# Performance work log

Hardware: AMD Instinct MI355X
Metric: run time of the kernel (lower is better)

The kernel has to match this reference:

```python
import jax, jax.numpy as jnp
import numpy as np

N_NODES, N_EDGES, BATCH_SIZE = 8192, 65536, 64
N_S, NG, MAX_R = 16, 32, 10.0
SQRT3 = float(np.sqrt(3.0))


def _mlp2(h, w1, b1, w2, b2):
    return jax.nn.relu(h @ w1 + b1) @ w2 + b2


def _mlp3(h, w1, b1, w2, b2, w3, b3):
    h = jax.nn.relu(h @ w1 + b1)
    h = jax.nn.relu(h @ w2 + b2)
    return h @ w3 + b3


def _scatter_mean(vals, idx, n):
    s = jax.ops.segment_sum(vals, idx, num_segments=n)
    c = jax.ops.segment_sum(jnp.ones(vals.shape[:1], vals.dtype), idx, num_segments=n)
    return s / jnp.maximum(c, 1.0)[:, None]


def _forward_molecule(x, pos, src, dst, batch, params):
    (ne_w1, ne_b1, ne_w2, ne_b2, ee_w1, ee_b1, ee_w2, ee_b2,
     c0_w1, c0_b1, c0_w2, c0_b2, c1_w1, c1_b1, c1_w2, c1_b2,
     sn_w1, sn_b1, sn_w2, sn_b2, sn_w3, sn_b3,
     se_w1, se_b1, se_w2, se_b2, se_w3, se_b3) = params
    n = x.shape[0]
    evec = pos[dst] - pos[src]                       # [E,3]
    dist = jnp.sqrt(jnp.sum(evec * evec, -1) + 1e-12)
    mu = jnp.linspace(0.0, MAX_R, NG)
    coeff = -0.5 / (MAX_R / (NG - 1)) ** 2           # GaussianSmearing
    edge_attr = jnp.exp(coeff * (dist[:, None] - mu) ** 2)     # [E,NG]
    sh1 = SQRT3 * evec / dist[:, None]               # l=1 SH, component norm; l=0 part == 1

    h = _mlp2(x, ne_w1, ne_b1, ne_w2, ne_b2)         # node embedding [N,16]
    eemb = _mlp2(edge_attr, ee_w1, ee_b1, ee_w2, ee_b2)        # edge embedding [E,16]

    # ---- conv 0: 16x0e (x) 0e+1o -> 16x0e+16x1o, per-edge TP weights ----
    ea = jnp.concatenate([eemb, h[dst, :N_S], h[src, :N_S]], -1)   # [E,48]
    w = _mlp2(ea, c0_w1, c0_b1, c0_w2, c0_b2)                      # [E,512]
    E = w.shape[0]
    w00 = w[:, :256].reshape(E, 16, 16)    # 0e x 0e -> 0e
    w01 = w[:, 256:].reshape(E, 16, 16)    # 0e x 1o -> 1o
    xs = h[src]
    o0 = 0.25 * jnp.einsum('eu,euw->ew', xs, w00)        # path weight 1/sqrt(16)
    o1 = 0.25 * jnp.einsum('eu,em,euw->ewm', xs, sh1, w01)
    tp = jnp.concatenate([o0, o1.reshape(E, 48)], -1)
    up = _scatter_mean(tp, dst, n)                       # [N,64]
    h = jnp.pad(h, ((0, 0), (0, up.shape[1] - h.shape[1]))) + up

    # ---- conv 1: 16x0e+16x1o (x) 0e+1o -> 16x0e+16x1o+16x1e ----
    ea = jnp.concatenate([eemb, h[dst, :N_S], h[src, :N_S]], -1)
    w = _mlp2(ea, c1_w1, c1_b1, c1_w2, c1_b2)                      # [E,1280]
    wA, wB, wC, wD, wE = (w[:, i * 256:(i + 1) * 256].reshape(E, 16, 16) for i in range(5))
    x0s = h[src, :16]
    x1s = h[src, 16:64].reshape(E, 16, 3)
    pw = 1.0 / float(np.sqrt(32.0))        # two fan-16 paths into 0e and into 1o
    o0 = pw * (jnp.einsum('eu,euw->ew', x0s, wA)
               + jnp.einsum('eui,ei,euw->ew', x1s, sh1, wD) / SQRT3)  # CG(1,1,0)=delta/sqrt3
    o1o = pw * (jnp.einsum('eu,em,euw->ewm', x0s, sh1, wB)
                + jnp.einsum('eum,euw->ewm', x1s, wC))
    cr = jnp.cross(x1s, sh1[:, None, :])                              # CG(1,1,1)=eps/sqrt2
    o1e = (0.25 / float(np.sqrt(2.0))) * jnp.einsum('euk,euw->ewk', cr, wE)
    tp = jnp.concatenate([o0, o1o.reshape(E, 48), o1e.reshape(E, 48)], -1)
    up = _scatter_mean(tp, dst, n)                       # [N,112]
    h = jnp.pad(h, ((0, 0), (0, up.shape[1] - h.shape[1]))) + up

    xf = h[:, :N_S]                                      # n_conv_layers < 3 branch
    s_nodes = _mlp3(xf, sn_w1, sn_b1, sn_w2, sn_b2, sn_w3, sn_b3)   # [N,1]
    s_edges = _mlp3(jnp.concatenate([edge_attr, xf[src], xf[dst]], -1),
                    se_w1, se_b1, se_w2, se_b2, se_w3, se_b3)       # [E,1]
    # edge_in_score=True -> edge and node scatter_add into per-molecule score
    return (jax.ops.segment_sum(s_edges, batch[src], num_segments=BATCH_SIZE)
            + jax.ops.segment_sum(s_nodes, batch, num_segments=BATCH_SIZE))


def setup_inputs() -> dict:
    ks = iter(jax.random.split(jax.random.key(0), 64))

    def nrm(shape, scale=1.0):
        return scale * jax.random.normal(next(ks), shape, jnp.float32)

    def lin(fi, fo):
        return nrm((fi, fo), 1.0 / float(np.sqrt(fi)))

    def z(n):
        return jnp.zeros((n,), jnp.float32)

    inp = {}
    for tag in ('r', 'p'):
        inp[f'x_{tag}'] = nrm((N_NODES, 32))
        inp[f'pos_{tag}'] = 2.0 * jax.random.normal(next(ks), (N_NODES, 3), jnp.float32)
        s = jax.random.randint(next(ks), (N_EDGES,), 0, N_NODES)
        o = jax.random.randint(next(ks), (N_EDGES,), 1, N_NODES)   # no self loops
        inp[f'edge_index_{tag}'] = jnp.stack([s, (s + o) % N_NODES]).astype(jnp.int32)
        inp[f'batch_{tag}'] = jnp.sort(jax.random.randint(next(ks), (N_NODES,), 0, BATCH_SIZE)).astype(jnp.int32)
    inp['ne_w1'] = lin(32, 16); inp['ne_b1'] = z(16); inp['ne_w2'] = lin(16, 16); inp['ne_b2'] = z(16)
    inp['ee_w1'] = lin(32, 16); inp['ee_b1'] = z(16); inp['ee_w2'] = lin(16, 16); inp['ee_b2'] = z(16)
    inp['c0_w1'] = lin(48, 48); inp['c0_b1'] = z(48); inp['c0_w2'] = lin(48, 512); inp['c0_b2'] = z(512)
    inp['c1_w1'] = lin(48, 48); inp['c1_b1'] = z(48); inp['c1_w2'] = lin(48, 1280); inp['c1_b2'] = z(1280)
    inp['sn_w1'] = lin(16, 32); inp['sn_b1'] = z(32); inp['sn_w2'] = lin(32, 16); inp['sn_b2'] = z(16)
    inp['sn_w3'] = lin(16, 1); inp['sn_b3'] = z(1)
    inp['se_w1'] = lin(64, 16); inp['se_b1'] = z(16); inp['se_w2'] = lin(16, 16); inp['se_b2'] = z(16)
    inp['se_w3'] = lin(16, 1); inp['se_b3'] = z(1)
    return inp


def reference(x_r, pos_r, edge_index_r, batch_r, x_p, pos_p, edge_index_p, batch_p,
              ne_w1, ne_b1, ne_w2, ne_b2, ee_w1, ee_b1, ee_w2, ee_b2,
              c0_w1, c0_b1, c0_w2, c0_b2, c1_w1, c1_b1, c1_w2, c1_b2,
              sn_w1, sn_b1, sn_w2, sn_b2, sn_w3, sn_b3,
              se_w1, se_b1, se_w2, se_b2, se_w3, se_b3):
    params = (ne_w1, ne_b1, ne_w2, ne_b2, ee_w1, ee_b1, ee_w2, ee_b2,
              c0_w1, c0_b1, c0_w2, c0_b2, c1_w1, c1_b1, c1_w2, c1_b2,
              sn_w1, sn_b1, sn_w2, sn_b2, sn_w3, sn_b3,
              se_w1, se_b1, se_w2, se_b2, se_w3, se_b3)
    e_r = _forward_molecule(x_r, pos_r, edge_index_r[0], edge_index_r[1], batch_r, params)
    e_p = _forward_molecule(x_p, pos_p, edge_index_p[0], edge_index_p[1], batch_p, params)
    return e_p - e_r   # reaction energy [BATCH_SIZE, 1]
```

## Files before the change

### kernel.cpp

```cpp
#include <hip/hip_runtime.h>
#include <math.h>

#define NN 8192
#define NE 65536
#define SQRT3F 1.7320508075688772f
#define INV_SQRT3F 0.5773502691896258f
#define PW 0.17677669529663687f
#define GSTEP (10.0f/31.0f)
#define GCOEFF (-0.5f/(GSTEP*GSTEP))

typedef _Float16 f16;
typedef f16 f16x2 __attribute__((ext_vector_type(2)));
typedef f16 f16x4 __attribute__((ext_vector_type(4)));
typedef f16 f16x8 __attribute__((ext_vector_type(8)));
typedef float f32x4 __attribute__((ext_vector_type(4)));

#define MFMA(acc, a, b) acc = __builtin_amdgcn_mfma_f32_16x16x32_f16(a, b, acc, 0, 0, 0)

__global__ __launch_bounds__(256) void k_pre(const float* __restrict__ c0w1, const float* __restrict__ c0b1,
                                             const float* __restrict__ c1w1, const float* __restrict__ c1b1,
                                             const float* __restrict__ c0w2, const float* __restrict__ c0b2,
                                             const float* __restrict__ c1w2, const float* __restrict__ c1b2,
                                             f16* __restrict__ w1c0, f16* __restrict__ w1c1,
                                             f16* __restrict__ w2t0, f16* __restrict__ w2t1,
                                             const float* __restrict__ xr, const float* __restrict__ xp,
                                             float* __restrict__ h16f, f16* __restrict__ h16_16,
                                             const float* __restrict__ nw1, const float* __restrict__ nb1,
                                             const float* __restrict__ nw2, const float* __restrict__ nb2,
                                             const int* __restrict__ eir, const int* __restrict__ eip,
                                             const float* __restrict__ posr, const float* __restrict__ posp,
                                             float* __restrict__ sh1d, f16* __restrict__ eemb16,
                                             int* __restrict__ cnt,
                                             const float* __restrict__ ew1, const float* __restrict__ eb1,
                                             const float* __restrict__ ew2, const float* __restrict__ eb2) {
    int b = blockIdx.x;
    int tid = threadIdx.x;
    if (b < 320) {
        int idx = b * 256 + tid;
        if (idx >= 1280 * 64) return;
        int n = idx >> 6, h = idx & 63;
        w2t1[idx] = (f16)((h < 48) ? c1w2[h * 1280 + n] : (h == 48 ? c1b2[n] : 0.f));
        if (n < 512) w2t0[idx] = (f16)((h < 48) ? c0w2[h * 512 + n] : (h == 48 ? c0b2[n] : 0.f));
        if (n < 48) {
            w1c0[idx] = (f16)((h < 48) ? c0w1[h * 48 + n] : (h == 48 ? c0b1[n] : 0.f));
            w1c1[idx] = (f16)((h < 48) ? c1w1[h * 48 + n] : (h == 48 ? c1b1[n] : 0.f));
        }
    } else if (b < 384) {
        int bb = b - 320;
        int mol = bb >> 5;
        const float* x = mol ? xp : xr;
        float* hf = h16f + (size_t)mol * NN * 16;
        f16* h16o = h16_16 + (size_t)mol * NN * 16;
        int v = (bb & 31) * 256 + tid;
        float xi[32];
#pragma unroll
        for (int i = 0; i < 32; i++) xi[i] = x[v * 32 + i];
        float a[16];
#pragma unroll
        for (int j = 0; j < 16; j++) a[j] = nb1[j];
#pragma unroll
        for (int i = 0; i < 32; i++)
#pragma unroll
            for (int j = 0; j < 16; j++) a[j] = fmaf(xi[i], nw1[i * 16 + j], a[j]);
#pragma unroll
        for (int j = 0; j < 16; j++) a[j] = fmaxf(a[j], 0.f);
        float o[16];
#pragma unroll
        for (int j = 0; j < 16; j++) o[j] = nb2[j];
#pragma unroll
        for (int i = 0; i < 16; i++)
#pragma unroll
            for (int j = 0; j < 16; j++) o[j] = fmaf(a[i], nw2[i * 16 + j], o[j]);
#pragma unroll
        for (int j = 0; j < 16; j++) { hf[v * 16 + j] = o[j]; h16o[v * 16 + j] = (f16)o[j]; }
    } else {
        int bb = b - 384;
        int mol = bb >> 8;
        const int* ei = mol ? eip : eir;
        const float* pos = mol ? posp : posr;
        float* sh_ = sh1d + (size_t)mol * NE * 4;
        f16* em_ = eemb16 + (size_t)mol * NE * 16;
        int* cn_ = cnt + mol * NN;
        int e = (bb & 255) * 256 + tid;
        int s = ei[e], d = ei[NE + e];
        float ex = pos[d * 3 + 0] - pos[s * 3 + 0];
        float ey = pos[d * 3 + 1] - pos[s * 3 + 1];
        float ez = pos[d * 3 + 2] - pos[s * 3 + 2];
        float dist = sqrtf(ex * ex + ey * ey + ez * ez + 1e-12f);
        float inv = SQRT3F / dist;
        sh_[e * 4 + 0] = ex * inv;
        sh_[e * 4 + 1] = ey * inv;
        sh_[e * 4 + 2] = ez * inv;
        sh_[e * 4 + 3] = dist;
        float g[32];
#pragma unroll
        for (int i = 0; i < 32; i++) {
            float t = dist - (float)i * GSTEP;
            g[i] = __expf(GCOEFF * t * t);
        }
        float a[16];
#pragma unroll
        for (int j = 0; j < 16; j++) a[j] = eb1[j];
#pragma unroll
        for (int i = 0; i < 32; i++)
#pragma unroll
            for (int j = 0; j < 16; j++) a[j] = fmaf(g[i], ew1[i * 16 + j], a[j]);
#pragma unroll
        for (int j = 0; j < 16; j++) a[j] = fmaxf(a[j], 0.f);
        float o[16];
#pragma unroll
        for (int j = 0; j < 16; j++) o[j] = eb2[j];
#pragma unroll
        for (int i = 0; i < 16; i++)
#pragma unroll
            for (int j = 0; j < 16; j++) o[j] = fmaf(a[i], ew2[i * 16 + j], o[j]);
#pragma unroll
        for (int j = 0; j < 16; j++) em_[e * 16 + j] = (f16)o[j];
        atomicAdd(&cn_[d], 1);
    }
}

__global__ __launch_bounds__(256) void k_scan(int* __restrict__ cnt, int* __restrict__ rowptr,
                                              float* __restrict__ out) {
    __shared__ int part[256];
    int mol = blockIdx.x;
    int* c = cnt + mol * NN;
    int* rp = rowptr + mol * (NN + 1);
    int t = threadIdx.x;
    int base = t * (NN / 256);
    int s = 0;
#pragma unroll
    for (int i = 0; i < NN / 256; i++) s += c[base + i];
    part[t] = s;
    __syncthreads();
    if (t == 0) {
        int run = 0;
        for (int i = 0; i < 256; i++) { int v = part[i]; part[i] = run; run += v; }
    }
    __syncthreads();
    int run = part[t];
    for (int i = 0; i < NN / 256; i++) {
        int cv = c[base + i];
        rp[base + i] = run;
        run += cv;
        c[base + i] = 0;
    }
    if (t == 255) rp[NN] = run;
    if (mol == 0 && t < 64) out[t] = 0.f;
}

__global__ __launch_bounds__(256) void k_fill(const int* __restrict__ eir, const int* __restrict__ eip,
                                              const int* __restrict__ rowptr, int* __restrict__ cnt,
                                              int* __restrict__ eord) {
    int mol = blockIdx.y;
    const int* ei = mol ? eip : eir;
    int e = blockIdx.x * 256 + threadIdx.x;
    int d = ei[NE + e];
    int pos = atomicAdd(&cnt[mol * NN + d], 1);
    eord[mol * NE + rowptr[mol * (NN + 1) + d] + pos] = e;
}

__global__ __launch_bounds__(128) void k_conv0(const int* __restrict__ eir, const int* __restrict__ eip,
                                               const int* __restrict__ eord,
                                               const f16* __restrict__ eemb16, const f16* __restrict__ h16_16,
                                               const float* __restrict__ sh1d,
                                               const f16* __restrict__ w1h, const f16* __restrict__ w2h,
                                               float* __restrict__ tp0) {
    __shared__ __align__(16) f16 ea[128 * 72];
    __shared__ __align__(16) f16 sc0[128 * 24];
    __shared__ __align__(16) float4 shs[128];
    int mol = blockIdx.y;
    const int* ei = mol ? eip : eir;
    const int* eo = eord + mol * NE;
    const f16* em_ = eemb16 + (size_t)mol * NE * 16;
    const f16* h16_ = h16_16 + (size_t)mol * NN * 16;
    const float* sh_ = sh1d + (size_t)mol * NE * 4;
    float* tp_ = tp0 + (size_t)mol * NE * 64;
    int tid = threadIdx.x;
    int e0 = blockIdx.x * 128;
    {
        int er = tid;
        int le = eo[e0 + er];
        int s = ei[le], d = ei[NE + le];
        char* row = (char*)ea + er * 144;
        const f16x8* pe = (const f16x8*)(em_ + (size_t)le * 16);
        ((f16x8*)row)[0] = pe[0]; ((f16x8*)row)[1] = pe[1];
        const f16x8* pd = (const f16x8*)(h16_ + (size_t)d * 16);
        ((f16x8*)row)[2] = pd[0]; ((f16x8*)row)[3] = pd[1];
        const f16x8* ps = (const f16x8*)(h16_ + (size_t)s * 16);
        f16x8 sv0 = ps[0], sv1 = ps[1];
        ((f16x8*)row)[4] = sv0; ((f16x8*)row)[5] = sv1;
        f16x8 z = {}; f16x8 o = {}; o[0] = (f16)1.0f;
        ((f16x8*)row)[6] = o; ((f16x8*)row)[7] = z; ((f16x8*)row)[8] = z;
        char* srow = (char*)sc0 + er * 48;
        *(f16x8*)srow = sv0;
        *(f16x8*)(srow + 16) = sv1;
        shs[er] = *(const float4*)(sh_ + (size_t)le * 4);
    }
    int wv = tid >> 6, l = tid & 63;
    int koff = (l >> 4) * 16;
    int voffB = (l & 15) * 128 + koff;
    int rbase = wv * 64;
#pragma unroll
    for (int t = 0; t < 4; t++) {
        int arow = rbase + t * 16 + (l & 15);
        f16x8 a0 = *(const f16x8*)((const char*)ea + arow * 144 + koff);
        f16x8 a1 = *(const f16x8*)((const char*)ea + arow * 144 + koff + 64);
#pragma unroll
        for (int nt = 0; nt < 3; nt++) {
            f32x4 hacc = {0.f, 0.f, 0.f, 0.f};
            const char* hb = (const char*)w1h + nt * 2048 + voffB;
            MFMA(hacc, a0, *(const f16x8*)(hb));
            MFMA(hacc, a1, *(const f16x8*)(hb + 64));
#pragma unroll
            for (int r = 0; r < 4; r++) {
                int rr = rbase + t * 16 + (l >> 4) * 4 + r;
                ea[rr * 72 + nt * 16 + (l & 15)] = (f16)fmaxf(hacc[r], 0.f);
            }
        }
    }
    f16x8 ha0[4], ha1[4];
#pragma unroll
    for (int t = 0; t < 4; t++) {
        int arow = rbase + t * 16 + (l & 15);
        ha0[t] = *(const f16x8*)((const char*)ea + arow * 144 + koff);
        ha1[t] = *(const f16x8*)((const char*)ea + arow * 144 + koff + 64);
    }
    f32x4 accA[4] = {}, accB[4] = {};
    const char* wB = (const char*)w2h + voffB;
    f16x8 cA0 = *(const f16x8*)(wB), cA1 = *(const f16x8*)(wB + 64);
    f16x8 cB0 = *(const f16x8*)(wB + 32768), cB1 = *(const f16x8*)(wB + 32768 + 64);
#pragma unroll 4
    for (int u = 0; u < 16; ++u) {
        int un = (u < 15) ? u + 1 : 15;
        const char* Hb = wB + un * 2048;
        f16x8 nA0 = *(const f16x8*)(Hb), nA1 = *(const f16x8*)(Hb + 64);
        f16x8 nB0 = *(const f16x8*)(Hb + 32768), nB1 = *(const f16x8*)(Hb + 32768 + 64);
#pragma unroll
        for (int t = 0; t < 4; t++) {
            f16 s = *(const f16*)((const char*)sc0 + (rbase + t * 16 + (l & 15)) * 48 + u * 2);
            f16x8 x0 = ha0[t] * s, x1 = ha1[t] * s;
            MFMA(accA[t], x0, cA0); MFMA(accA[t], x1, cA1);
            MFMA(accB[t], x0, cB0); MFMA(accB[t], x1, cB1);
        }
        cA0 = nA0; cA1 = nA1; cB0 = nB0; cB1 = nB1;
    }
    int w = l & 15;
#pragma unroll
    for (int t = 0; t < 4; t++)
#pragma unroll
        for (int r = 0; r < 4; r++) {
            int ro = rbase + t * 16 + (l >> 4) * 4 + r;
            int i = e0 + ro;
            float4 shv = shs[ro];
            float* tpp = tp_ + (size_t)i * 64;
            float tb = 0.25f * accB[t][r];
            tpp[w] = 0.25f * accA[t][r];
            tpp[16 + w] = tb * shv.x;
            tpp[32 + w] = tb * shv.y;
            tpp[48 + w] = tb * shv.z;
        }
}

__global__ __launch_bounds__(256) void k_up0g(const float* __restrict__ h16f, const float* __restrict__ tp0,
                                              const int* __restrict__ rowptr,
                                              float* __restrict__ h64f, f16* __restrict__ h64_16) {
    int mol = blockIdx.y;
    const float* h_ = h16f + (size_t)mol * NN * 16;
    const float* tp = tp0 + (size_t)mol * NE * 64;
    const int* rp = rowptr + mol * (NN + 1);
    float* o_ = h64f + (size_t)mol * NN * 64;
    f16* o16_ = h64_16 + (size_t)mol * NN * 16;
    int tid = threadIdx.x;
    int v = blockIdx.x * 64 + (tid >> 2), q = tid & 3;
    int r0 = rp[v], r1 = rp[v + 1];
    float acc[16];
#pragma unroll
    for (int j = 0; j < 16; j++) acc[j] = 0.f;
    for (int i = r0; i < r1; i++) {
        const float4* src = (const float4*)(tp + (size_t)i * 64 + q * 16);
#pragma unroll
        for (int j2 = 0; j2 < 4; j2++) {
            float4 vv = src[j2];
            acc[j2 * 4 + 0] += vv.x; acc[j2 * 4 + 1] += vv.y;
            acc[j2 * 4 + 2] += vv.z; acc[j2 * 4 + 3] += vv.w;
        }
    }
    float rc = 1.0f / fmaxf((float)(r1 - r0), 1.0f);
    if (q == 0) {
#pragma unroll
        for (int w = 0; w < 16; w++) {
            float val = fmaf(acc[w], rc, h_[(size_t)v * 16 + w]);
            o_[(size_t)v * 64 + w] = val;
            o16_[(size_t)v * 16 + w] = (f16)val;
        }
    } else {
#pragma unroll
        for (int w = 0; w < 16; w++) o_[(size_t)v * 64 + 16 + 3 * w + (q - 1)] = acc[w] * rc;
    }
}

__global__ __launch_bounds__(128) void k_conv1(const int* __restrict__ eir, const int* __restrict__ eip,
                                               const int* __restrict__ eord,
                                               const f16* __restrict__ eemb16, const f16* __restrict__ h64_16,
                                               const float* __restrict__ h64f, const float* __restrict__ sh1d,
                                               const f16* __restrict__ w1h, const f16* __restrict__ w2h,
                                               float* __restrict__ tp1) {
    __shared__ __align__(16) f16 ea[128 * 72];
    __shared__ __align__(16) f16 sc1[128 * 36];
    int mol = blockIdx.y;
    const int* ei = mol ? eip : eir;
    const int* eo = eord + mol * NE;
    const f16* em_ = eemb16 + (size_t)mol * NE * 16;
    const f16* h16_ = h64_16 + (size_t)mol * NN * 16;
    const float* hf_ = h64f + (size_t)mol * NN * 64;
    const float* sh_ = sh1d + (size_t)mol * NE * 4;
    float* tp_ = tp1 + (size_t)mol * NE * 16;
    int tid = threadIdx.x;
    int e0 = blockIdx.x * 128;
    {
        int er = tid;
        int le = eo[e0 + er];
        int s = ei[le], d = ei[NE + le];
        char* row = (char*)ea + er * 144;
        const f16x8* pe = (const f16x8*)(em_ + (size_t)le * 16);
        ((f16x8*)row)[0] = pe[0]; ((f16x8*)row)[1] = pe[1];
        const f16x8* pd = (const f16x8*)(h16_ + (size_t)d * 16);
        ((f16x8*)row)[2] = pd[0]; ((f16x8*)row)[3] = pd[1];
        const f16x8* ps = (const f16x8*)(h16_ + (size_t)s * 16);
        ((f16x8*)row)[4] = ps[0]; ((f16x8*)row)[5] = ps[1];
        f16x8 z = {}; f16x8 o = {}; o[0] = (f16)1.0f;
        ((f16x8*)row)[6] = o; ((f16x8*)row)[7] = z; ((f16x8*)row)[8] = z;
        float4 shv = *(const float4*)(sh_ + (size_t)le * 4);
        const float* hfs = hf_ + (size_t)s * 64;
        float xu[16];
#pragma unroll
        for (int g = 0; g < 4; g++) {
            float4 v4 = *(const float4*)(hfs + g * 4);
            xu[g * 4 + 0] = v4.x; xu[g * 4 + 1] = v4.y; xu[g * 4 + 2] = v4.z; xu[g * 4 + 3] = v4.w;
        }
        float x1v[48];
#pragma unroll
        for (int g = 0; g < 12; g++) {
            float4 v4 = *(const float4*)(hfs + 16 + g * 4);
            x1v[g * 4 + 0] = v4.x; x1v[g * 4 + 1] = v4.y; x1v[g * 4 + 2] = v4.z; x1v[g * 4 + 3] = v4.w;
        }
        char* srow = (char*)sc1 + er * 72;
#pragma unroll
        for (int g = 0; g < 4; g++) {
            f16x8 pk;
#pragma unroll
            for (int k2 = 0; k2 < 4; k2++) {
                int k = g * 4 + k2;
                float du = (x1v[k * 3] * shv.x + x1v[k * 3 + 1] * shv.y + x1v[k * 3 + 2] * shv.z) * INV_SQRT3F;
                pk[k2 * 2 + 0] = (f16)xu[k];
                pk[k2 * 2 + 1] = (f16)du;
            }
            *(f16x8*)(srow + g * 16) = pk;
        }
    }
    int wv = tid >> 6, l = tid & 63;
    int koff = (l >> 4) * 16;
    int voffB = (l & 15) * 128 + koff;
    int rbase = wv * 64;
#pragma unroll
    for (int t = 0; t < 4; t++) {
        int arow = rbase + t * 16 + (l & 15);
        f16x8 a0 = *(const f16x8*)((const char*)ea + arow * 144 + koff);
        f16x8 a1 = *(const f16x8*)((const char*)ea + arow * 144 + koff + 64);
#pragma unroll
        for (int nt = 0; nt < 3; nt++) {
            f32x4 hacc = {0.f, 0.f, 0.f, 0.f};
            const char* hb = (const char*)w1h + nt * 2048 + voffB;
            MFMA(hacc, a0, *(const f16x8*)(hb));
            MFMA(hacc, a1, *(const f16x8*)(hb + 64));
#pragma unroll
            for (int r = 0; r < 4; r++) {
                int rr = rbase + t * 16 + (l >> 4) * 4 + r;
                ea[rr * 72 + nt * 16 + (l & 15)] = (f16)fmaxf(hacc[r], 0.f);
            }
        }
    }
    f16x8 ha0[4], ha1[4];
#pragma unroll
    for (int t = 0; t < 4; t++) {
        int arow = rbase + t * 16 + (l & 15);
        ha0[t] = *(const f16x8*)((const char*)ea + arow * 144 + koff);
        ha1[t] = *(const f16x8*)((const char*)ea + arow * 144 + koff + 64);
    }
    f32x4 accA[4] = {};
    const char* wB = (const char*)w2h + voffB;
    f16x8 cA0 = *(const f16x8*)(wB), cA1 = *(const f16x8*)(wB + 64);
    f16x8 cD0 = *(const f16x8*)(wB + 98304), cD1 = *(const f16x8*)(wB + 98304 + 64);
#pragma unroll 4
    for (int u = 0; u < 16; ++u) {
        int un = (u < 15) ? u + 1 : 15;
        const char* Hb = wB + un * 2048;
        f16x8 nA0 = *(const f16x8*)(Hb), nA1 = *(const f16x8*)(Hb + 64);
        f16x8 nD0 = *(const f16x8*)(Hb + 98304), nD1 = *(const f16x8*)(Hb + 98304 + 64);
#pragma unroll
        for (int t = 0; t < 4; t++) {
            f16x2 sp = *(const f16x2*)((const char*)sc1 + (rbase + t * 16 + (l & 15)) * 72 + u * 4);
            f16x8 x0 = ha0[t] * sp[0], x1 = ha1[t] * sp[0];
            MFMA(accA[t], x0, cA0); MFMA(accA[t], x1, cA1);
            x0 = ha0[t] * sp[1]; x1 = ha1[t] * sp[1];
            MFMA(accA[t], x0, cD0); MFMA(accA[t], x1, cD1);
        }
        cA0 = nA0; cA1 = nA1; cD0 = nD0; cD1 = nD1;
    }
    int w = l & 15;
#pragma unroll
    for (int t = 0; t < 4; t++)
#pragma unroll
        for (int r = 0; r < 4; r++) {
            int i = e0 + rbase + t * 16 + (l >> 4) * 4 + r;
            tp_[(size_t)i * 16 + w] = PW * accA[t][r];
        }
}

__global__ __launch_bounds__(256) void k_xfg(const float* __restrict__ h64f, const float* __restrict__ tp1,
                                             const int* __restrict__ rowptr,
                                             float* __restrict__ xf,
                                             const int* __restrict__ batchr, const int* __restrict__ batchp,
                                             const float* __restrict__ w1, const float* __restrict__ b1,
                                             const float* __restrict__ w2, const float* __restrict__ b2,
                                             const float* __restrict__ w3, const float* __restrict__ b3,
                                             float* __restrict__ out) {
    __shared__ float xfs[64][17];
    __shared__ float buck[64];
    int tid = threadIdx.x;
    if (tid < 64) buck[tid] = 0.f;
    int mol = blockIdx.y;
    float sign = mol ? 1.f : -1.f;
    const int* batch = mol ? batchp : batchr;
    const float* h_ = h64f + (size_t)mol * NN * 64;
    const float* tp = tp1 + (size_t)mol * NE * 16;
    const int* rp = rowptr + mol * (NN + 1);
    float* xf_ = xf + (size_t)mol * NN * 16;
    int v = blockIdx.x * 64 + (tid >> 2), q = tid & 3;
    int r0 = rp[v], r1 = rp[v + 1];
    float a0 = 0.f, a1 = 0.f, a2 = 0.f, a3 = 0.f;
    for (int i = r0; i < r1; i++) {
        float4 t4 = *(const float4*)(tp + (size_t)i * 16 + q * 4);
        a0 += t4.x; a1 += t4.y; a2 += t4.z; a3 += t4.w;
    }
    float rc = 1.0f / fmaxf((float)(r1 - r0), 1.0f);
    float4 hv = *(const float4*)(h_ + (size_t)v * 64 + q * 4);
    float4 xv4;
    xv4.x = fmaf(a0, rc, hv.x); xv4.y = fmaf(a1, rc, hv.y);
    xv4.z = fmaf(a2, rc, hv.z); xv4.w = fmaf(a3, rc, hv.w);
    xfs[tid >> 2][q * 4 + 0] = xv4.x; xfs[tid >> 2][q * 4 + 1] = xv4.y;
    xfs[tid >> 2][q * 4 + 2] = xv4.z; xfs[tid >> 2][q * 4 + 3] = xv4.w;
    *(float4*)(xf_ + (size_t)v * 16 + q * 4) = xv4;
    __syncthreads();
    if (tid < 64) {
        int v2 = blockIdx.x * 64 + tid;
        float xv[16];
#pragma unroll
        for (int c = 0; c < 16; c++) xv[c] = xfs[tid][c];
        float aa[32];
#pragma unroll
        for (int j = 0; j < 32; j++) aa[j] = b1[j];
#pragma unroll
        for (int i = 0; i < 16; i++)
#pragma unroll
            for (int j = 0; j < 32; j++) aa[j] = fmaf(xv[i], w1[i * 32 + j], aa[j]);
#pragma unroll
        for (int j = 0; j < 32; j++) aa[j] = fmaxf(aa[j], 0.f);
        float bb[16];
#pragma unroll
        for (int j = 0; j < 16; j++) bb[j] = b2[j];
#pragma unroll
        for (int i = 0; i < 32; i++)
#pragma unroll
            for (int j = 0; j < 16; j++) bb[j] = fmaf(aa[i], w2[i * 16 + j], bb[j]);
#pragma unroll
        for (int j = 0; j < 16; j++) bb[j] = fmaxf(bb[j], 0.f);
        float val = b3[0];
#pragma unroll
        for (int i = 0; i < 16; i++) val = fmaf(bb[i], w3[i], val);
        atomicAdd(&buck[batch[v2]], val);
    }
    __syncthreads();
    if (tid < 64) atomicAdd(&out[tid], sign * buck[tid]);
}

__global__ __launch_bounds__(256) void k_sedge(const int* __restrict__ eir, const int* __restrict__ eip,
                                               const int* __restrict__ batchr, const int* __restrict__ batchp,
                                               const float* __restrict__ sh1d, const float* __restrict__ xf,
                                               const float* __restrict__ w1, const float* __restrict__ b1,
                                               const float* __restrict__ w2, const float* __restrict__ b2,
                                               const float* __restrict__ w3, const float* __restrict__ b3,
                                               float* __restrict__ out) {
    __shared__ float buck[64];
    int tid = threadIdx.x;
    if (tid < 64) buck[tid] = 0.f;
    __syncthreads();
    int mol = blockIdx.y;
    float sign = mol ? 1.f : -1.f;
    const int* ei = mol ? eip : eir;
    const int* batch = mol ? batchp : batchr;
    const float* sh_ = sh1d + (size_t)mol * NE * 4;
    const float* xf_ = xf + (size_t)mol * NN * 16;
    int e = blockIdx.x * 256 + tid;
    int s = ei[e], d = ei[NE + e];
    float dist = sh_[e * 4 + 3];
    float in[64];
#pragma unroll
    for (int i = 0; i < 32; i++) {
        float t = dist - (float)i * GSTEP;
        in[i] = __expf(GCOEFF * t * t);
    }
#pragma unroll
    for (int i = 0; i < 16; i++) in[32 + i] = xf_[s * 16 + i];
#pragma unroll
    for (int i = 0; i < 16; i++) in[48 + i] = xf_[d * 16 + i];
    float a[16];
#pragma unroll
    for (int j = 0; j < 16; j++) a[j] = b1[j];
#pragma unroll
    for (int i = 0; i < 64; i++)
#pragma unroll
        for (int j = 0; j < 16; j++) a[j] = fmaf(in[i], w1[i * 16 + j], a[j]);
#pragma unroll
    for (int j = 0; j < 16; j++) a[j] = fmaxf(a[j], 0.f);
    float bb[16];
#pragma unroll
    for (int j = 0; j < 16; j++) bb[j] = b2[j];
#pragma unroll
    for (int i = 0; i < 16; i++)
#pragma unroll
        for (int j = 0; j < 16; j++) bb[j] = fmaf(a[i], w2[i * 16 + j], bb[j]);
#pragma unroll
    for (int j = 0; j < 16; j++) bb[j] = fmaxf(bb[j], 0.f);
    float val = b3[0];
#pragma unroll
    for (int i = 0; i < 16; i++) val = fmaf(bb[i], w3[i], val);
    atomicAdd(&buck[batch[s]], val);
    __syncthreads();
    if (tid < 64) atomicAdd(&out[tid], sign * buck[tid]);
}

extern "C" void kernel_launch(void* const* d_in, const int* in_sizes, int n_in,
                              void* d_out, int out_size, void* d_ws, size_t ws_size,
                              hipStream_t stream) {
    const float* x_r = (const float*)d_in[0];
    const float* pos_r = (const float*)d_in[1];
    const int* ei_r = (const int*)d_in[2];
    const int* batch_r = (const int*)d_in[3];
    const float* x_p = (const float*)d_in[4];
    const float* pos_p = (const float*)d_in[5];
    const int* ei_p = (const int*)d_in[6];
    const int* batch_p = (const int*)d_in[7];
    const float* ne_w1 = (const float*)d_in[8];
    const float* ne_b1 = (const float*)d_in[9];
    const float* ne_w2 = (const float*)d_in[10];
    const float* ne_b2 = (const float*)d_in[11];
    const float* ee_w1 = (const float*)d_in[12];
    const float* ee_b1 = (const float*)d_in[13];
    const float* ee_w2 = (const float*)d_in[14];
    const float* ee_b2 = (const float*)d_in[15];
    const float* c0_w1 = (const float*)d_in[16];
    const float* c0_b1 = (const float*)d_in[17];
    const float* c0_w2 = (const float*)d_in[18];
    const float* c0_b2 = (const float*)d_in[19];
    const float* c1_w1 = (const float*)d_in[20];
    const float* c1_b1 = (const float*)d_in[21];
    const float* c1_w2 = (const float*)d_in[22];
    const float* c1_b2 = (const float*)d_in[23];
    const float* sn_w1 = (const float*)d_in[24];
    const float* sn_b1 = (const float*)d_in[25];
    const float* sn_w2 = (const float*)d_in[26];
    const float* sn_b2 = (const float*)d_in[27];
    const float* sn_w3 = (const float*)d_in[28];
    const float* sn_b3 = (const float*)d_in[29];
    const float* se_w1 = (const float*)d_in[30];
    const float* se_b1 = (const float*)d_in[31];
    const float* se_w2 = (const float*)d_in[32];
    const float* se_b2 = (const float*)d_in[33];
    const float* se_w3 = (const float*)d_in[34];
    const float* se_b3 = (const float*)d_in[35];
    float* out = (float*)d_out;

    char* p = (char*)d_ws;
    auto alloc = [&](size_t bytes) { char* r = p; p += (bytes + 255) & ~(size_t)255; return r; };
    f16* w2t1 = (f16*)alloc(1280 * 64 * 2);
    f16* w2t0 = (f16*)alloc(512 * 64 * 2);
    f16* w1c0 = (f16*)alloc(48 * 64 * 2);
    f16* w1c1 = (f16*)alloc(48 * 64 * 2);
    f16* eemb16 = (f16*)alloc((size_t)2 * NE * 16 * 2);
    f16* h16_16 = (f16*)alloc((size_t)2 * NN * 16 * 2);
    f16* h64_16 = (f16*)alloc((size_t)2 * NN * 16 * 2);
    float* h16f = (float*)alloc((size_t)2 * NN * 16 * 4);
    float* sh1d = (float*)alloc((size_t)2 * NE * 4 * 4);
    int* cntI = (int*)alloc((size_t)2 * NN * 4);
    int* rowptr = (int*)alloc((size_t)2 * (NN + 1) * 4);
    int* eord = (int*)alloc((size_t)2 * NE * 4);
    float* tp0 = (float*)alloc((size_t)2 * NE * 64 * 4);
    float* tp1 = tp0;
    float* h64f = (float*)alloc((size_t)2 * NN * 64 * 4);
    float* xf = (float*)alloc((size_t)2 * NN * 16 * 4);
    (void)ws_size; (void)n_in; (void)in_sizes; (void)out_size;

    hipMemsetAsync(cntI, 0, (size_t)2 * NN * 4, stream);

    dim3 blk256(256, 1, 1), blk128(128, 1, 1);
    dim3 ge(NE / 256, 2, 1);
    dim3 gc(NE / 128, 2, 1);

    k_pre<<<dim3(896, 1, 1), blk256, 0, stream>>>(c0_w1, c0_b1, c1_w1, c1_b1, c0_w2, c0_b2, c1_w2, c1_b2,
                                                  w1c0, w1c1, w2t0, w2t1,
                                                  x_r, x_p, h16f, h16_16, ne_w1, ne_b1, ne_w2, ne_b2,
                                                  ei_r, ei_p, pos_r, pos_p, sh1d, eemb16, cntI,
                                                  ee_w1, ee_b1, ee_w2, ee_b2);
    k_scan<<<dim3(2, 1, 1), blk256, 0, stream>>>(cntI, rowptr, out);
    k_fill<<<ge, blk256, 0, stream>>>(ei_r, ei_p, rowptr, cntI, eord);
    k_conv0<<<gc, blk128, 0, stream>>>(ei_r, ei_p, eord, eemb16, h16_16, sh1d, w1c0, w2t0, tp0);
    k_up0g<<<dim3(NN / 64, 2, 1), blk256, 0, stream>>>(h16f, tp0, rowptr, h64f, h64_16);
    k_conv1<<<gc, blk128, 0, stream>>>(ei_r, ei_p, eord, eemb16, h64_16, h64f, sh1d, w1c1, w2t1, tp1);
    k_xfg<<<dim3(NN / 64, 2, 1), blk256, 0, stream>>>(h64f, tp1, rowptr, xf, batch_r, batch_p,
                                                      sn_w1, sn_b1, sn_w2, sn_b2, sn_w3, sn_b3, out);
    k_sedge<<<ge, blk256, 0, stream>>>(ei_r, ei_p, batch_r, batch_p, sh1d, xf,
                                       se_w1, se_b1, se_w2, se_b2, se_w3, se_b3, out);
}
```

Measured before the change: 152.7 us.

## Store conv tensor-product outputs in fp16 and double edges per conv block

The per-edge tensor-product buffers tp0/tp1 are now written and read as fp16 rather than fp32, which halves the intermediate traffic between the conv kernels and the segment-mean kernels. Each conv block now handles 256 edges with 128 threads: every wave processes 8 row tiles, so weight fragments are reused across twice as many edges and the grid shrinks by half. The cost is more registers and LDS per block, which may lower occupancy, and fp16 rounding of the intermediates before the fp32 accumulation.

```diff
diff --git a/kernel.cpp b/kernel.cpp
--- a/kernel.cpp
+++ b/kernel.cpp
@@ -165,21 +165,22 @@
                                                const f16* __restrict__ eemb16, const f16* __restrict__ h16_16,
                                                const float* __restrict__ sh1d,
                                                const f16* __restrict__ w1h, const f16* __restrict__ w2h,
-                                               float* __restrict__ tp0) {
-    __shared__ __align__(16) f16 ea[128 * 72];
-    __shared__ __align__(16) f16 sc0[128 * 24];
-    __shared__ __align__(16) float4 shs[128];
+                                               f16* __restrict__ tp0) {
+    __shared__ __align__(16) f16 ea[256 * 72];
+    __shared__ __align__(16) f16 sc0[256 * 24];
+    __shared__ __align__(16) float4 shs[256];
     int mol = blockIdx.y;
     const int* ei = mol ? eip : eir;
     const int* eo = eord + mol * NE;
     const f16* em_ = eemb16 + (size_t)mol * NE * 16;
     const f16* h16_ = h16_16 + (size_t)mol * NN * 16;
     const float* sh_ = sh1d + (size_t)mol * NE * 4;
-    float* tp_ = tp0 + (size_t)mol * NE * 64;
+    f16* tp_ = tp0 + (size_t)mol * NE * 64;
     int tid = threadIdx.x;
-    int e0 = blockIdx.x * 128;
-    {
-        int er = tid;
+    int e0 = blockIdx.x * 256;
+#pragma unroll
+    for (int ii = 0; ii < 2; ii++) {
+        int er = tid * 2 + ii;
         int le = eo[e0 + er];
         int s = ei[le], d = ei[NE + le];
         char* row = (char*)ea + er * 144;
@@ -200,9 +201,9 @@
     int wv = tid >> 6, l = tid & 63;
     int koff = (l >> 4) * 16;
     int voffB = (l & 15) * 128 + koff;
-    int rbase = wv * 64;
-#pragma unroll
-    for (int t = 0; t < 4; t++) {
+    int rbase = wv * 128;
+#pragma unroll
+    for (int t = 0; t < 8; t++) {
         int arow = rbase + t * 16 + (l & 15);
         f16x8 a0 = *(const f16x8*)((const char*)ea + arow * 144 + koff);
         f16x8 a1 = *(const f16x8*)((const char*)ea + arow * 144 + koff + 64);
@@ -219,14 +220,14 @@
             }
         }
     }
-    f16x8 ha0[4], ha1[4];
-#pragma unroll
-    for (int t = 0; t < 4; t++) {
+    f16x8 ha0[8], ha1[8];
+#pragma unroll
+    for (int t = 0; t < 8; t++) {
         int arow = rbase + t * 16 + (l & 15);
         ha0[t] = *(const f16x8*)((const char*)ea + arow * 144 + koff);
         ha1[t] = *(const f16x8*)((const char*)ea + arow * 144 + koff + 64);
     }
-    f32x4 accA[4] = {}, accB[4] = {};
+    f32x4 accA[8] = {}, accB[8] = {};
     const char* wB = (const char*)w2h + voffB;
     f16x8 cA0 = *(const f16x8*)(wB), cA1 = *(const f16x8*)(wB + 64);
     f16x8 cB0 = *(const f16x8*)(wB + 32768), cB1 = *(const f16x8*)(wB + 32768 + 64);
@@ -237,7 +238,7 @@
         f16x8 nA0 = *(const f16x8*)(Hb), nA1 = *(const f16x8*)(Hb + 64);
         f16x8 nB0 = *(const f16x8*)(Hb + 32768), nB1 = *(const f16x8*)(Hb + 32768 + 64);
 #pragma unroll
-        for (int t = 0; t < 4; t++) {
+        for (int t = 0; t < 8; t++) {
             f16 s = *(const f16*)((const char*)sc0 + (rbase + t * 16 + (l & 15)) * 48 + u * 2);
             f16x8 x0 = ha0[t] * s, x1 = ha1[t] * s;
             MFMA(accA[t], x0, cA0); MFMA(accA[t], x1, cA1);
@@ -247,27 +248,27 @@
     }
     int w = l & 15;
 #pragma unroll
-    for (int t = 0; t < 4; t++)
+    for (int t = 0; t < 8; t++)
 #pragma unroll
         for (int r = 0; r < 4; r++) {
             int ro = rbase + t * 16 + (l >> 4) * 4 + r;
             int i = e0 + ro;
             float4 shv = shs[ro];
-            float* tpp = tp_ + (size_t)i * 64;
+            f16* tpp = tp_ + (size_t)i * 64;
             float tb = 0.25f * accB[t][r];
-            tpp[w] = 0.25f * accA[t][r];
-            tpp[16 + w] = tb * shv.x;
-            tpp[32 + w] = tb * shv.y;
-            tpp[48 + w] = tb * shv.z;
-        }
-}
-
-__global__ __launch_bounds__(256) void k_up0g(const float* __restrict__ h16f, const float* __restrict__ tp0,
+            tpp[w] = (f16)(0.25f * accA[t][r]);
+            tpp[16 + w] = (f16)(tb * shv.x);
+            tpp[32 + w] = (f16)(tb * shv.y);
+            tpp[48 + w] = (f16)(tb * shv.z);
+        }
+}
+
+__global__ __launch_bounds__(256) void k_up0g(const float* __restrict__ h16f, const f16* __restrict__ tp0,
                                               const int* __restrict__ rowptr,
                                               float* __restrict__ h64f, f16* __restrict__ h64_16) {
     int mol = blockIdx.y;
     const float* h_ = h16f + (size_t)mol * NN * 16;
-    const float* tp = tp0 + (size_t)mol * NE * 64;
+    const f16* tp = tp0 + (size_t)mol * NE * 64;
     const int* rp = rowptr + mol * (NN + 1);
     float* o_ = h64f + (size_t)mol * NN * 64;
     f16* o16_ = h64_16 + (size_t)mol * NN * 16;
@@ -278,13 +279,11 @@
 #pragma unroll
     for (int j = 0; j < 16; j++) acc[j] = 0.f;
     for (int i = r0; i < r1; i++) {
-        const float4* src = (const float4*)(tp + (size_t)i * 64 + q * 16);
-#pragma unroll
-        for (int j2 = 0; j2 < 4; j2++) {
-            float4 vv = src[j2];
-            acc[j2 * 4 + 0] += vv.x; acc[j2 * 4 + 1] += vv.y;
-            acc[j2 * 4 + 2] += vv.z; acc[j2 * 4 + 3] += vv.w;
-        }
+        const f16* src = tp + (size_t)i * 64 + q * 16;
+        f16x8 v0 = *(const f16x8*)src;
+        f16x8 v1 = *(const f16x8*)(src + 8);
+#pragma unroll
+        for (int j = 0; j < 8; j++) { acc[j] += (float)v0[j]; acc[8 + j] += (float)v1[j]; }
     }
     float rc = 1.0f / fmaxf((float)(r1 - r0), 1.0f);
     if (q == 0) {
@@ -305,9 +304,9 @@
                                                const f16* __restrict__ eemb16, const f16* __restrict__ h64_16,
                                                const float* __restrict__ h64f, const float* __restrict__ sh1d,
                                                const f16* __restrict__ w1h, const f16* __restrict__ w2h,
-                                               float* __restrict__ tp1) {
-    __shared__ __align__(16) f16 ea[128 * 72];
-    __shared__ __align__(16) f16 sc1[128 * 36];
+                                               f16* __restrict__ tp1) {
+    __shared__ __align__(16) f16 ea[256 * 72];
+    __shared__ __align__(16) f16 sc1[256 * 36];
     int mol = blockIdx.y;
     const int* ei = mol ? eip : eir;
     const int* eo = eord + mol * NE;
@@ -315,11 +314,12 @@
     const f16* h16_ = h64_16 + (size_t)mol * NN * 16;
     const float* hf_ = h64f + (size_t)mol * NN * 64;
     const float* sh_ = sh1d + (size_t)mol * NE * 4;
-    float* tp_ = tp1 + (size_t)mol * NE * 16;
+    f16* tp_ = tp1 + (size_t)mol * NE * 16;
     int tid = threadIdx.x;
-    int e0 = blockIdx.x * 128;
-    {
-        int er = tid;
+    int e0 = blockIdx.x * 256;
+#pragma unroll
+    for (int ii = 0; ii < 2; ii++) {
+        int er = tid * 2 + ii;
         int le = eo[e0 + er];
         int s = ei[le], d = ei[NE + le];
         char* row = (char*)ea + er * 144;
@@ -362,9 +362,9 @@
     int wv = tid >> 6, l = tid & 63;
     int koff = (l >> 4) * 16;
     int voffB = (l & 15) * 128 + koff;
-    int rbase = wv * 64;
-#pragma unroll
-    for (int t = 0; t < 4; t++) {
+    int rbase = wv * 128;
+#pragma unroll
+    for (int t = 0; t < 8; t++) {
         int arow = rbase + t * 16 + (l & 15);
         f16x8 a0 = *(const f16x8*)((const char*)ea + arow * 144 + koff);
         f16x8 a1 = *(const f16x8*)((const char*)ea + arow * 144 + koff + 64);
@@ -381,14 +381,14 @@
             }
         }
     }
-    f16x8 ha0[4], ha1[4];
-#pragma unroll
-    for (int t = 0; t < 4; t++) {
+    f16x8 ha0[8], ha1[8];
+#pragma unroll
+    for (int t = 0; t < 8; t++) {
         int arow = rbase + t * 16 + (l & 15);
         ha0[t] = *(const f16x8*)((const char*)ea + arow * 144 + koff);
         ha1[t] = *(const f16x8*)((const char*)ea + arow * 144 + koff + 64);
     }
-    f32x4 accA[4] = {};
+    f32x4 accA[8] = {};
     const char* wB = (const char*)w2h + voffB;
     f16x8 cA0 = *(const f16x8*)(wB), cA1 = *(const f16x8*)(wB + 64);
     f16x8 cD0 = *(const f16x8*)(wB + 98304), cD1 = *(const f16x8*)(wB + 98304 + 64);
@@ -399,7 +399,7 @@
         f16x8 nA0 = *(const f16x8*)(Hb), nA1 = *(const f16x8*)(Hb + 64);
         f16x8 nD0 = *(const f16x8*)(Hb + 98304), nD1 = *(const f16x8*)(Hb + 98304 + 64);
 #pragma unroll
-        for (int t = 0; t < 4; t++) {
+        for (int t = 0; t < 8; t++) {
             f16x2 sp = *(const f16x2*)((const char*)sc1 + (rbase + t * 16 + (l & 15)) * 72 + u * 4);
             f16x8 x0 = ha0[t] * sp[0], x1 = ha1[t] * sp[0];
             MFMA(accA[t], x0, cA0); MFMA(accA[t], x1, cA1);
@@ -410,15 +410,15 @@
     }
     int w = l & 15;
 #pragma unroll
-    for (int t = 0; t < 4; t++)
+    for (int t = 0; t < 8; t++)
 #pragma unroll
         for (int r = 0; r < 4; r++) {
             int i = e0 + rbase + t * 16 + (l >> 4) * 4 + r;
-            tp_[(size_t)i * 16 + w] = PW * accA[t][r];
-        }
-}
-
-__global__ __launch_bounds__(256) void k_xfg(const float* __restrict__ h64f, const float* __restrict__ tp1,
+            tp_[(size_t)i * 16 + w] = (f16)(PW * accA[t][r]);
+        }
+}
+
+__global__ __launch_bounds__(256) void k_xfg(const float* __restrict__ h64f, const f16* __restrict__ tp1,
                                              const int* __restrict__ rowptr,
                                              float* __restrict__ xf,
                                              const int* __restrict__ batchr, const int* __restrict__ batchp,
@@ -434,15 +434,15 @@
     float sign = mol ? 1.f : -1.f;
     const int* batch = mol ? batchp : batchr;
     const float* h_ = h64f + (size_t)mol * NN * 64;
-    const float* tp = tp1 + (size_t)mol * NE * 16;
+    const f16* tp = tp1 + (size_t)mol * NE * 16;
     const int* rp = rowptr + mol * (NN + 1);
     float* xf_ = xf + (size_t)mol * NN * 16;
     int v = blockIdx.x * 64 + (tid >> 2), q = tid & 3;
     int r0 = rp[v], r1 = rp[v + 1];
     float a0 = 0.f, a1 = 0.f, a2 = 0.f, a3 = 0.f;
     for (int i = r0; i < r1; i++) {
-        float4 t4 = *(const float4*)(tp + (size_t)i * 16 + q * 4);
-        a0 += t4.x; a1 += t4.y; a2 += t4.z; a3 += t4.w;
+        f16x4 t4 = *(const f16x4*)(tp + (size_t)i * 16 + q * 4);
+        a0 += (float)t4[0]; a1 += (float)t4[1]; a2 += (float)t4[2]; a3 += (float)t4[3];
     }
     float rc = 1.0f / fmaxf((float)(r1 - r0), 1.0f);
     float4 hv = *(const float4*)(h_ + (size_t)v * 64 + q * 4);
@@ -596,8 +596,8 @@
     int* cntI = (int*)alloc((size_t)2 * NN * 4);
     int* rowptr = (int*)alloc((size_t)2 * (NN + 1) * 4);
     int* eord = (int*)alloc((size_t)2 * NE * 4);
-    float* tp0 = (float*)alloc((size_t)2 * NE * 64 * 4);
-    float* tp1 = tp0;
+    f16* tp0 = (f16*)alloc((size_t)2 * NE * 64 * 2);
+    f16* tp1 = tp0;
     float* h64f = (float*)alloc((size_t)2 * NN * 64 * 4);
     float* xf = (float*)alloc((size_t)2 * NN * 16 * 4);
     (void)ws_size; (void)n_in; (void)in_sizes; (void)out_size;
@@ -606,7 +606,7 @@
 
     dim3 blk256(256, 1, 1), blk128(128, 1, 1);
     dim3 ge(NE / 256, 2, 1);
-    dim3 gc(NE / 128, 2, 1);
+    dim3 gc(NE / 256, 2, 1);
 
     k_pre<<<dim3(896, 1, 1), blk256, 0, stream>>>(c0_w1, c0_b1, c1_w1, c1_b1, c0_w2, c0_b2, c1_w2, c1_b2,
                                                   w1c0, w1c1, w2t0, w2t1,
```

Result: faster. 147.8 us (-3.2%).
